# Kernel optimization log

Measured on AMD Instinct MI355X. Metric: run time of the kernel, lower is better.

The kernel has to match this reference:

```python
import jax, jax.numpy as jnp
import numpy as np

B, C, H, W = 32, 3, 224, 224
P = 14            # n_patches per side
PS = H // P       # 16
D = 768           # hidden_d
NH = 12           # n_heads
HD = D // NH      # 64
L = 12            # n_blocks
DFF = 4 * D
OUT = 1000
S = P * P + 1     # 197 tokens
EPS = 1e-5


def layernorm(x, g, b):
    m = jnp.mean(x, axis=-1, keepdims=True)
    v = jnp.mean(jnp.square(x - m), axis=-1, keepdims=True)
    return (x - m) * jax.lax.rsqrt(v + EPS) * g + b


def setup_inputs() -> dict:
    key = jax.random.key(0)
    ks = jax.random.split(key, 16)
    w = lambda k, shape: (jax.random.normal(k, shape, jnp.float32) * 0.02)
    inp = {
        'x': jax.random.normal(ks[0], (B, C, H, W), jnp.float32),
        'emb_w': w(ks[1], (C * PS * PS, D)),
        'emb_b': jnp.zeros((D,), jnp.float32),
        'cls': w(ks[2], (1, D)),
        'pos': w(ks[3], (S, D)),
        'pre_g': jnp.ones((D,), jnp.float32),
        'pre_b': jnp.zeros((D,), jnp.float32),
        'ln1_g': jnp.ones((L, D), jnp.float32),
        'ln1_b': jnp.zeros((L, D), jnp.float32),
        'qkv_w': w(ks[4], (L, D, 3 * D)),
        'qkv_b': jnp.zeros((L, 3 * D), jnp.float32),
        'proj_w': w(ks[5], (L, D, D)),
        'proj_b': jnp.zeros((L, D), jnp.float32),
        'ln2_g': jnp.ones((L, D), jnp.float32),
        'ln2_b': jnp.zeros((L, D), jnp.float32),
        'fc1_w': w(ks[6], (L, D, DFF)),
        'fc1_b': jnp.zeros((L, DFF), jnp.float32),
        'fc2_w': w(ks[7], (L, DFF, D)),
        'fc2_b': jnp.zeros((L, D), jnp.float32),
        'post_g': jnp.ones((D,), jnp.float32),
        'post_b': jnp.zeros((D,), jnp.float32),
        'head1_w': w(ks[8], (D, D)),
        'head1_b': jnp.zeros((D,), jnp.float32),
        'head2_w': w(ks[9], (D, OUT)),
        'head2_b': jnp.zeros((OUT,), jnp.float32),
    }
    return inp


def _forward(x, emb_w, emb_b, cls, pos, pre_g, pre_b,
             ln1_g, ln1_b, qkv_w, qkv_b, proj_w, proj_b,
             ln2_g, ln2_b, fc1_w, fc1_b, fc2_w, fc2_b,
             post_g, post_b, head1_w, head1_b, head2_w, head2_b):
    n = x.shape[0]
    # patchify: [n,C,H,W] -> [n, P*P, C*PS*PS] with flatten order (c, ph, pw)
    patches = x.reshape(n, C, P, PS, P, PS)
    patches = patches.transpose(0, 2, 4, 1, 3, 5).reshape(n, P * P, C * PS * PS)
    tokens = patches @ emb_w + emb_b                      # [n, P*P, D]
    tokens = jnp.concatenate([jnp.broadcast_to(cls[None], (n, 1, D)), tokens], axis=1)
    h = layernorm(tokens + pos[None], pre_g, pre_b)       # [n, S, D]

    scale = 1.0 / np.sqrt(HD)

    def block(h, p):
        g1, b1, qw, qb, pw, pb, g2, b2, f1w, f1b, f2w, f2b = p
        y = layernorm(h, g1, b1)
        qkv = (y @ qw + qb).reshape(n, S, 3, NH, HD).transpose(2, 0, 3, 1, 4)
        q, k, v = qkv[0], qkv[1], qkv[2]                  # [n, NH, S, HD]
        scores = jnp.einsum('bhsd,bhtd->bhst', q, k) * scale
        attn = jax.nn.softmax(scores, axis=-1)
        ctx = jnp.einsum('bhst,bhtd->bhsd', attn, v)
        ctx = ctx.transpose(0, 2, 1, 3).reshape(n, S, D)
        h = h + ctx @ pw + pb
        y = layernorm(h, g2, b2)
        mlp = jax.nn.gelu(y @ f1w + f1b, approximate=False) @ f2w + f2b
        return h + mlp, None

    h, _ = jax.lax.scan(block, h,
                        (ln1_g, ln1_b, qkv_w, qkv_b, proj_w, proj_b,
                         ln2_g, ln2_b, fc1_w, fc1_b, fc2_w, fc2_b))

    cls_out = layernorm(h[:, 0, :], post_g, post_b)
    preds = jnp.tanh(cls_out @ head1_w + head1_b) @ head2_w + head2_b
    return preds


def reference(x, emb_w, emb_b, cls, pos, pre_g, pre_b,
              ln1_g, ln1_b, qkv_w, qkv_b, proj_w, proj_b,
              ln2_g, ln2_b, fc1_w, fc1_b, fc2_w, fc2_b,
              post_g, post_b, head1_w, head1_b, head2_w, head2_b):
    return _forward(x, emb_w, emb_b, cls, pos, pre_g, pre_b,
                    ln1_g, ln1_b, qkv_w, qkv_b, proj_w, proj_b,
                    ln2_g, ln2_b, fc1_w, fc1_b, fc2_w, fc2_b,
                    post_g, post_b, head1_w, head1_b, head2_w, head2_b)
```

## Files before the change

### kernel.cpp

```cpp
#include <hip/hip_runtime.h>
#include <hip/hip_bf16.h>
#include <math.h>
#include <cstdint>

constexpr int Bn   = 32;
constexpr int Dn   = 768;
constexpr int NHn  = 12;
constexpr int HDn  = 64;
constexpr int Ln   = 12;
constexpr int DFFn = 3072;
constexpr int OUTn = 1000;
constexpr int Sn   = 197;
constexpr int Mrows = Bn * Sn;
constexpr int NPATCH = 196;

typedef __attribute__((ext_vector_type(8))) short bf16x8;
typedef __attribute__((ext_vector_type(4))) float f32x4;

__device__ inline void store_val(float* p, float v) { *p = v; }
__device__ inline void store_val(__hip_bfloat16* p, float v) { *p = __float2bfloat16(v); }
__device__ inline short f2bs(float f) {
  __hip_bfloat16 h = __float2bfloat16(f);
  return __builtin_bit_cast(short, h);
}

__device__ inline void gload_lds16(const void* g, void* l) {
  auto gp = (const __attribute__((address_space(1))) unsigned int*)(uintptr_t)g;
  auto lp = (__attribute__((address_space(3))) unsigned int*)(uintptr_t)l;
  __builtin_amdgcn_global_load_lds(gp, lp, 16, 0, 0);
}

__device__ inline int xcd_swizzle(int orig, int nwg) {
  const int xcd = orig & 7, local = orig >> 3;
  const int q = nwg >> 3, r = nwg & 7;
  return (xcd < r) ? xcd * (q + 1) + local : r * (q + 1) + (xcd - r) * q + local;
}

template<int ACT, bool RES, typename OT>
__global__ __launch_bounds__(256) void bgemm_kernel(
    const __hip_bfloat16* __restrict__ A,
    const __hip_bfloat16* __restrict__ Bt,
    const float* __restrict__ bias,
    const float* __restrict__ res,
    OT* __restrict__ out, int M, int N, int K)
{
  __shared__ __hip_bfloat16 As[3][128 * 32];
  __shared__ __hip_bfloat16 Bs[3][128 * 32];
  const int tid  = threadIdx.x;
  const int w    = tid >> 6, lane = tid & 63;
  const int wm   = w >> 1,   wn   = w & 1;
  const int kg   = lane >> 4, fr = lane & 15;

  const int nwg = gridDim.x * gridDim.y;
  const int wg  = xcd_swizzle(blockIdx.y * gridDim.x + blockIdx.x, nwg);
  const int bm  = (wg / gridDim.x) * 128;
  const int bn  = (wg % gridDim.x) * 128;

  const int obase0 = w * 2048;
  const int obase1 = w * 2048 + 1024;
  const int o0 = obase0 + lane * 16, o1 = obase1 + lane * 16;
  const int r0 = o0 >> 6,            r1 = o1 >> 6;
  const int ks0 = (((o0 >> 4) & 3) ^ (r0 & 3)) * 8;
  const int ks1 = (((o1 >> 4) & 3) ^ (r1 & 3)) * 8;
  const int ga0 = (bm + r0 >= M) ? M - 1 : bm + r0;
  const int ga1 = (bm + r1 >= M) ? M - 1 : bm + r1;
  const int gb0 = bn + r0, gb1 = bn + r1;

  f32x4 acc[4][4];
  #pragma unroll
  for (int i = 0; i < 4; ++i)
    #pragma unroll
    for (int j = 0; j < 4; ++j) acc[i][j] = (f32x4)(0.f);

  const int nt = K >> 5;

  auto STAGE = [&](int t, int bi) {
    const int k0 = t << 5;
    gload_lds16(A  + (size_t)ga0 * K + k0 + ks0, (char*)As[bi] + obase0);
    gload_lds16(A  + (size_t)ga1 * K + k0 + ks1, (char*)As[bi] + obase1);
    gload_lds16(Bt + (size_t)gb0 * K + k0 + ks0, (char*)Bs[bi] + obase0);
    gload_lds16(Bt + (size_t)gb1 * K + k0 + ks1, (char*)Bs[bi] + obase1);
  };
  auto COMPUTE = [&](int bi) {
    bf16x8 af[4], bfv[4];
    #pragma unroll
    for (int tt = 0; tt < 4; ++tt) {
      const int r = wm * 64 + tt * 16 + fr;
      af[tt]  = *(const bf16x8*)((const char*)As[bi] + r * 64 + ((kg ^ (r & 3)) << 4));
      const int c = wn * 64 + tt * 16 + fr;
      bfv[tt] = *(const bf16x8*)((const char*)Bs[bi] + c * 64 + ((kg ^ (c & 3)) << 4));
    }
    #pragma unroll
    for (int mt = 0; mt < 4; ++mt)
      #pragma unroll
      for (int nt2 = 0; nt2 < 4; ++nt2)
        acc[mt][nt2] = __builtin_amdgcn_mfma_f32_16x16x32_bf16(af[mt], bfv[nt2], acc[mt][nt2], 0, 0, 0);
  };

  STAGE(0, 0);
  STAGE(1, 1);

  int cur = 0;
  for (int t = 0; t < nt - 1; ++t) {
    asm volatile("s_waitcnt vmcnt(4)" ::: "memory");
    __builtin_amdgcn_s_barrier();
    __builtin_amdgcn_sched_barrier(0);
    if (t + 2 < nt) {
      int nb = cur + 2; if (nb >= 3) nb -= 3;
      STAGE(t + 2, nb);
    }
    COMPUTE(cur);
    ++cur; if (cur == 3) cur = 0;
  }
  asm volatile("s_waitcnt vmcnt(0)" ::: "memory");
  __builtin_amdgcn_s_barrier();
  __builtin_amdgcn_sched_barrier(0);
  COMPUTE(cur);

  #pragma unroll
  for (int nt2 = 0; nt2 < 4; ++nt2) {
    const int cb = bn + wn * 64 + nt2 * 16 + fr;
    const float bs = bias[cb];
    #pragma unroll
    for (int mt = 0; mt < 4; ++mt) {
      #pragma unroll
      for (int j = 0; j < 4; ++j) {
        const int rb = bm + wm * 64 + mt * 16 + kg * 4 + j;
        if (rb >= M) continue;
        float v = acc[mt][nt2][j] + bs;
        if (ACT == 1) v = 0.5f * v * (1.f + erff(v * 0.70710678118654752f));
        if (RES) v += res[(size_t)rb * N + cb];
        store_val(out + (size_t)rb * N + cb, v);
      }
    }
  }
}

template<int ACT, bool RES, typename OT>
__global__ __launch_bounds__(512) void wgemm_kernel(
    const __hip_bfloat16* __restrict__ A,
    const __hip_bfloat16* __restrict__ Bt,
    const float* __restrict__ bias,
    const float* __restrict__ res,
    OT* __restrict__ out, int M, int N, int K)
{
  constexpr int BUFSZ = 24576;
  __shared__ __align__(16) char lds[3 * BUFSZ];
  const int tid  = threadIdx.x;
  const int wid  = tid >> 6, lane = tid & 63;
  const int wm   = wid >> 2, wn = wid & 3;
  const int kg   = lane >> 4, fr = lane & 15;
  const int rs   = lane >> 2;
  const int ks   = (((lane & 3) ^ ((lane >> 2) & 3)) << 3);

  const int gx  = gridDim.x;
  const int nwg = gx * gridDim.y;
  const int wg  = xcd_swizzle(blockIdx.y * gx + blockIdx.x, nwg);
  const int bm  = (wg / gx) * 128;
  const int bn  = (wg % gx) * 256;

  f32x4 acc[4][4];
  #pragma unroll
  for (int i = 0; i < 4; ++i)
    #pragma unroll
    for (int j = 0; j < 4; ++j) acc[i][j] = (f32x4)(0.f);

  const int nt = K >> 5;

  auto STAGE = [&](int t) {
    const int k0 = t << 5;
    char* buf = lds + (t % 3) * BUFSZ;
    #pragma unroll
    for (int j = 0; j < 3; ++j) {
      const int c = wid + j * 8;
      const __hip_bfloat16* src;
      if (c < 8) {
        int gr = bm + c * 16 + rs; if (gr >= M) gr = M - 1;
        src = A + (size_t)gr * K + k0 + ks;
      } else {
        const int gc = bn + (c - 8) * 16 + rs;
        src = Bt + (size_t)gc * K + k0 + ks;
      }
      gload_lds16(src, buf + c * 1024);
    }
  };
  auto COMPUTE = [&](int t) {
    const char* buf = lds + (t % 3) * BUFSZ;
    bf16x8 af[4], bfv[4];
    #pragma unroll
    for (int tt = 0; tt < 4; ++tt) {
      const int r = wm * 64 + tt * 16 + fr;
      af[tt]  = *(const bf16x8*)(buf + r * 64 + ((kg ^ (r & 3)) << 4));
      const int c = wn * 64 + tt * 16 + fr;
      bfv[tt] = *(const bf16x8*)(buf + 8192 + c * 64 + ((kg ^ (c & 3)) << 4));
    }
    #pragma unroll
    for (int mt = 0; mt < 4; ++mt)
      #pragma unroll
      for (int nt2 = 0; nt2 < 4; ++nt2)
        acc[mt][nt2] = __builtin_amdgcn_mfma_f32_16x16x32_bf16(af[mt], bfv[nt2], acc[mt][nt2], 0, 0, 0);
  };

  STAGE(0);
  STAGE(1);

  for (int t = 0; t < nt - 1; ++t) {
    asm volatile("s_waitcnt vmcnt(3)" ::: "memory");
    __builtin_amdgcn_s_barrier();
    __builtin_amdgcn_sched_barrier(0);
    if (t + 2 < nt) STAGE(t + 2);
    COMPUTE(t);
  }
  asm volatile("s_waitcnt vmcnt(0)" ::: "memory");
  __builtin_amdgcn_s_barrier();
  __builtin_amdgcn_sched_barrier(0);
  COMPUTE(nt - 1);

  #pragma unroll
  for (int fj = 0; fj < 4; ++fj) {
    const int col = bn + wn * 64 + fj * 16 + fr;
    const float bs = bias[col];
    #pragma unroll
    for (int fi = 0; fi < 4; ++fi) {
      #pragma unroll
      for (int j = 0; j < 4; ++j) {
        const int row = bm + wm * 64 + fi * 16 + kg * 4 + j;
        if (row >= M) continue;
        float v = acc[fi][fj][j] + bs;
        if (ACT == 1) v = 0.5f * v * (1.f + erff(v * 0.70710678118654752f));
        if (RES) v += res[(size_t)row * N + col];
        store_val(out + (size_t)row * N + col, v);
      }
    }
  }
}

__global__ __launch_bounds__(256) void convT_kernel(const float* __restrict__ W,
                                                    __hip_bfloat16* __restrict__ Wt,
                                                    int K, int N)
{
  const size_t lw = (size_t)K * N;
  const float* Wb = W + blockIdx.z * lw;
  __hip_bfloat16* Wo = Wt + blockIdx.z * lw;
  __shared__ float t[32][33];
  const int k0 = blockIdx.y * 32, n0 = blockIdx.x * 32;
  const int r  = threadIdx.x >> 3, c4 = (threadIdx.x & 7) * 4;
  const float* wp = Wb + (size_t)(k0 + r) * N + n0 + c4;
  float4 v = make_float4(0.f, 0.f, 0.f, 0.f);
  if (n0 + c4 + 3 < N) v = *(const float4*)wp;
  else {
    if (n0 + c4 + 0 < N) v.x = wp[0];
    if (n0 + c4 + 1 < N) v.y = wp[1];
    if (n0 + c4 + 2 < N) v.z = wp[2];
  }
  t[r][c4 + 0] = v.x; t[r][c4 + 1] = v.y; t[r][c4 + 2] = v.z; t[r][c4 + 3] = v.w;
  __syncthreads();
  const int n = n0 + r;
  if (n < N) {
    __hip_bfloat16* o = Wo + (size_t)n * K + k0 + c4;
    o[0] = __float2bfloat16(t[c4 + 0][r]);
    o[1] = __float2bfloat16(t[c4 + 1][r]);
    o[2] = __float2bfloat16(t[c4 + 2][r]);
    o[3] = __float2bfloat16(t[c4 + 3][r]);
  }
}

template<int ACT>
__global__ __launch_bounds__(256) void hgemv_kernel(
    const float* __restrict__ A, const __hip_bfloat16* __restrict__ Wt,
    const float* __restrict__ bias, float* __restrict__ out, int N, int K)
{
  const int w = threadIdx.x >> 6, lane = threadIdx.x & 63;
  const int e = blockIdx.x * 4 + w;
  const int m = e & 31, n = e >> 5;
  if (n >= N) return;
  const float* a = A + (size_t)m * K;
  const __hip_bfloat16* wr = Wt + (size_t)n * K;
  float s = 0.f;
  for (int k = lane; k < K; k += 64)
    s = fmaf(a[k], __bfloat162float(wr[k]), s);
  #pragma unroll
  for (int o = 32; o > 0; o >>= 1) s += __shfl_xor(s, o);
  if (lane == 0) {
    float v = s + bias[n];
    if (ACT == 2) v = tanhf(v);
    out[(size_t)m * N + n] = v;
  }
}

__global__ __launch_bounds__(256) void patchify_kernel(const float* __restrict__ x,
                                                       __hip_bfloat16* __restrict__ p)
{
  size_t i = (size_t)blockIdx.x * 256 + threadIdx.x;
  constexpr size_t total = (size_t)Bn * NPATCH * 768;
  if (i >= total) return;
  int k = (int)(i % 768);
  size_t m = i / 768;
  int b = (int)(m / NPATCH), pp = (int)(m % NPATCH);
  int py = pp / 14, px = pp % 14;
  int c = k >> 8, ph = (k >> 4) & 15, pw = k & 15;
  p[i] = __float2bfloat16(x[(((size_t)(b * 3 + c)) * 224 + py * 16 + ph) * 224 + px * 16 + pw]);
}

__global__ __launch_bounds__(256) void assemble_kernel(const float* __restrict__ tok,
                                                       const float* __restrict__ cls,
                                                       const float* __restrict__ pos,
                                                       float* __restrict__ outp)
{
  size_t i = (size_t)blockIdx.x * 256 + threadIdx.x;
  constexpr size_t total = (size_t)Bn * Sn * Dn;
  if (i >= total) return;
  int d = (int)(i % Dn);
  size_t m = i / Dn;
  int s = (int)(m % Sn);
  size_t b = m / Sn;
  float v = (s == 0) ? cls[d] : tok[(b * NPATCH + (s - 1)) * Dn + d];
  outp[i] = v + pos[s * Dn + d];
}

template<typename OT>
__global__ __launch_bounds__(256) void ln_kernel(const float* __restrict__ x, size_t xstride,
                                                 const float* __restrict__ g,
                                                 const float* __restrict__ bt,
                                                 OT* __restrict__ out)
{
  const int row = blockIdx.x;
  const int tid = threadIdx.x;
  const float* xr = x + (size_t)row * xstride;
  float v0 = xr[tid], v1 = xr[tid + 256], v2 = xr[tid + 512];
  float s = v0 + v1 + v2;
  float q = v0 * v0 + v1 * v1 + v2 * v2;
  #pragma unroll
  for (int o = 32; o > 0; o >>= 1) { s += __shfl_down(s, o); q += __shfl_down(q, o); }
  __shared__ float sa[4], sb[4];
  int w = tid >> 6, lane = tid & 63;
  if (lane == 0) { sa[w] = s; sb[w] = q; }
  __syncthreads();
  if (tid == 0) {
    float ts = sa[0] + sa[1] + sa[2] + sa[3];
    float tq = sb[0] + sb[1] + sb[2] + sb[3];
    sa[0] = ts; sb[0] = tq;
  }
  __syncthreads();
  s = sa[0]; q = sb[0];
  const float mean = s * (1.f / 768.f);
  const float var  = q * (1.f / 768.f) - mean * mean;
  const float inv  = rsqrtf(var + 1e-5f);
  OT* orow = out + (size_t)row * Dn;
  store_val(orow + tid,       (v0 - mean) * inv * g[tid]       + bt[tid]);
  store_val(orow + tid + 256, (v1 - mean) * inv * g[tid + 256] + bt[tid + 256]);
  store_val(orow + tid + 512, (v2 - mean) * inv * g[tid + 512] + bt[tid + 512]);
}

constexpr int SP2 = 224;
constexpr int VTS = 232;
__global__ __launch_bounds__(256) void attn_mfma_kernel(
    const __hip_bfloat16* __restrict__ qkv, __hip_bfloat16* __restrict__ ctx)
{
  const int b = blockIdx.x / NHn, h = blockIdx.x % NHn;
  const int tid = threadIdx.x;
  const int w = tid >> 6, lane = tid & 63;
  const int kg = lane >> 4, fr = lane & 15;

  __shared__ short Kl[SP2 * 64];
  __shared__ short Vt[64 * VTS];
  __shared__ short Pl[4 * 2048];

  const size_t rstr = 3 * (size_t)Dn;
  const __hip_bfloat16* base = qkv + (size_t)b * Sn * rstr;

  #pragma unroll
  for (int it = 0; it < 7; ++it) {
    const int i = it * 256 + tid;
    const int r = i >> 3, s = i & 7;
    const int rr = r < Sn ? r : Sn - 1;
    gload_lds16(base + (size_t)rr * rstr + Dn + h * HDn + ((s ^ (r & 7)) << 3),
                (char*)Kl + it * 4096 + w * 1024);
  }
  #pragma unroll
  for (int it = 0; it < 7; ++it) {
    const int i = it * 256 + tid;
    const int key = i >> 3, d0 = (i & 7) * 8;
    const int rr = key < Sn ? key : Sn - 1;
    bf16x8 v = *(const bf16x8*)(base + (size_t)rr * rstr + 2 * Dn + h * HDn + d0);
    #pragma unroll
    for (int e = 0; e < 8; ++e) Vt[(d0 + e) * VTS + key] = v[e];
  }
  const int qw = w * 64;
  bf16x8 qf[4][2];
  #pragma unroll
  for (int qt = 0; qt < 4; ++qt)
    #pragma unroll
    for (int kk = 0; kk < 2; ++kk) {
      int q = qw + qt * 16 + fr; if (q >= Sn) q = Sn - 1;
      qf[qt][kk] = *(const bf16x8*)(base + (size_t)q * rstr + h * HDn + kk * 32 + kg * 8);
    }
  __syncthreads();

  float mold[4][4], lsum[4][4];
  f32x4 cacc[4][4];
  #pragma unroll
  for (int qt = 0; qt < 4; ++qt)
    #pragma unroll
    for (int j = 0; j < 4; ++j) {
      mold[qt][j] = -1e30f; lsum[qt][j] = 0.f;
      cacc[qt][j] = (f32x4)(0.f);
    }
  const float scale = 0.125f;

  for (int kc = 0; kc < SP2; kc += 32) {
    f32x4 sacc[4][2];
    #pragma unroll
    for (int qt = 0; qt < 4; ++qt) { sacc[qt][0] = (f32x4)(0.f); sacc[qt][1] = (f32x4)(0.f); }
    #pragma unroll
    for (int nt = 0; nt < 2; ++nt) {
      const int key = kc + nt * 16 + fr;
      const bf16x8 kf0 = *(const bf16x8*)((const char*)Kl + key * 128 + ((kg ^ (key & 7)) << 4));
      const bf16x8 kf1 = *(const bf16x8*)((const char*)Kl + key * 128 + (((4 + kg) ^ (key & 7)) << 4));
      #pragma unroll
      for (int qt = 0; qt < 4; ++qt) {
        sacc[qt][nt] = __builtin_amdgcn_mfma_f32_16x16x32_bf16(qf[qt][0], kf0, sacc[qt][nt], 0, 0, 0);
        sacc[qt][nt] = __builtin_amdgcn_mfma_f32_16x16x32_bf16(qf[qt][1], kf1, sacc[qt][nt], 0, 0, 0);
      }
    }
    const float madd0 = (kc + fr < Sn) ? 0.f : -3e38f;
    const float madd1 = (kc + 16 + fr < Sn) ? 0.f : -3e38f;
    #pragma unroll
    for (int qt = 0; qt < 4; ++qt) {
      sacc[qt][0] = sacc[qt][0] * scale + (f32x4)(madd0);
      sacc[qt][1] = sacc[qt][1] * scale + (f32x4)(madd1);
    }
    #pragma unroll
    for (int qt = 0; qt < 4; ++qt) {
      #pragma unroll
      for (int j = 0; j < 4; ++j) {
        float t = fmaxf(sacc[qt][0][j], sacc[qt][1][j]);
        t = fmaxf(t, __shfl_xor(t, 1));
        t = fmaxf(t, __shfl_xor(t, 2));
        t = fmaxf(t, __shfl_xor(t, 4));
        t = fmaxf(t, __shfl_xor(t, 8));
        const float mn = fmaxf(mold[qt][j], t);
        const float corr = __expf(mold[qt][j] - mn);
        mold[qt][j] = mn;
        const float p0 = __expf(sacc[qt][0][j] - mn);
        const float p1 = __expf(sacc[qt][1][j] - mn);
        sacc[qt][0][j] = p0; sacc[qt][1][j] = p1;
        float ps = p0 + p1;
        ps += __shfl_xor(ps, 1); ps += __shfl_xor(ps, 2);
        ps += __shfl_xor(ps, 4); ps += __shfl_xor(ps, 8);
        lsum[qt][j] = lsum[qt][j] * corr + ps;
        #pragma unroll
        for (int ht = 0; ht < 4; ++ht) cacc[qt][ht][j] *= corr;
      }
      #pragma unroll
      for (int nt = 0; nt < 2; ++nt) {
        const int c = nt * 16 + fr;
        #pragma unroll
        for (int j = 0; j < 4; ++j) {
          const int r = qt * 16 + kg * 4 + j;
          Pl[w * 2048 + r * 32 + (((c >> 3) ^ (r & 3)) << 3) + (c & 7)] = f2bs(sacc[qt][nt][j]);
        }
      }
    }
    bf16x8 vf[4];
    #pragma unroll
    for (int ht = 0; ht < 4; ++ht)
      vf[ht] = *(const bf16x8*)(Vt + (ht * 16 + fr) * VTS + kc + kg * 8);
    #pragma unroll
    for (int qt = 0; qt < 4; ++qt) {
      const int r = qt * 16 + fr;
      const bf16x8 pf = *(const bf16x8*)(Pl + w * 2048 + r * 32 + ((kg ^ (r & 3)) << 3));
      #pragma unroll
      for (int ht = 0; ht < 4; ++ht)
        cacc[qt][ht] = __builtin_amdgcn_mfma_f32_16x16x32_bf16(pf, vf[ht], cacc[qt][ht], 0, 0, 0);
    }
  }
  __hip_bfloat16* cb = ctx + (size_t)b * Sn * Dn + h * HDn;
  #pragma unroll
  for (int qt = 0; qt < 4; ++qt)
    #pragma unroll
    for (int j = 0; j < 4; ++j) {
      const int q = qw + qt * 16 + kg * 4 + j;
      if (q < Sn) {
        const float inv = 1.f / lsum[qt][j];
        #pragma unroll
        for (int ht = 0; ht < 4; ++ht)
          cb[(size_t)q * Dn + ht * 16 + fr] = __float2bfloat16(cacc[qt][ht][j] * inv);
      }
    }
}

using bf16 = __hip_bfloat16;

static inline void run_convT(const float* W, bf16* Wt, int K, int N, int L, hipStream_t st) {
  convT_kernel<<<dim3((N + 31) / 32, K / 32, L), 256, 0, st>>>(W, Wt, K, N);
}

extern "C" void kernel_launch(void* const* d_in, const int* in_sizes, int n_in,
                              void* d_out, int out_size, void* d_ws, size_t ws_size,
                              hipStream_t stream)
{
  const float* x      = (const float*)d_in[0];
  const float* emb_w  = (const float*)d_in[1];
  const float* emb_b  = (const float*)d_in[2];
  const float* cls    = (const float*)d_in[3];
  const float* pos    = (const float*)d_in[4];
  const float* pre_g  = (const float*)d_in[5];
  const float* pre_b  = (const float*)d_in[6];
  const float* ln1_g  = (const float*)d_in[7];
  const float* ln1_b  = (const float*)d_in[8];
  const float* qkv_w  = (const float*)d_in[9];
  const float* qkv_b  = (const float*)d_in[10];
  const float* proj_w = (const float*)d_in[11];
  const float* proj_b = (const float*)d_in[12];
  const float* ln2_g  = (const float*)d_in[13];
  const float* ln2_b  = (const float*)d_in[14];
  const float* fc1_w  = (const float*)d_in[15];
  const float* fc1_b  = (const float*)d_in[16];
  const float* fc2_w  = (const float*)d_in[17];
  const float* fc2_b  = (const float*)d_in[18];
  const float* post_g = (const float*)d_in[19];
  const float* post_b = (const float*)d_in[20];
  const float* h1_w   = (const float*)d_in[21];
  const float* h1_b   = (const float*)d_in[22];
  const float* h2_w   = (const float*)d_in[23];
  const float* h2_b   = (const float*)d_in[24];
  float* out = (float*)d_out;

  const size_t HN = (size_t)Mrows * Dn;
  float* hbuf = (float*)d_ws;
  bf16*  qkvb = (bf16*)(hbuf + HN);
  bf16*  abf1 = qkvb + (size_t)Mrows * 3 * Dn;
  bf16*  abf2 = abf1 + HN;
  bf16*  wtb  = abf2 + (size_t)Mrows * DFFn;

  bf16* bigq = wtb + (size_t)2304 * 768;
  bf16* bigp = bigq + (size_t)Ln * 3 * Dn * Dn;
  bf16* big1 = bigp + (size_t)Ln * Dn * Dn;
  bf16* big2 = big1 + (size_t)Ln * Dn * DFFn;
  const size_t need_big = (size_t)((char*)(big2 + (size_t)Ln * DFFn * Dn) - (char*)d_ws);
  const bool useBig = ws_size >= need_big;

  const int gM = (Mrows + 127) / 128;

  if (useBig) {
    run_convT(qkv_w,  bigq, Dn, 3 * Dn, Ln, stream);
    run_convT(proj_w, bigp, Dn, Dn,     Ln, stream);
    run_convT(fc1_w,  big1, Dn, DFFn,   Ln, stream);
    run_convT(fc2_w,  big2, DFFn, Dn,   Ln, stream);
  }

  patchify_kernel<<<(Bn * NPATCH * Dn) / 256, 256, 0, stream>>>(x, abf1);
  run_convT(emb_w, wtb, Dn, Dn, 1, stream);
  bgemm_kernel<0, false, float><<<dim3(Dn / 128, (Bn * NPATCH + 127) / 128), 256, 0, stream>>>(
      abf1, wtb, emb_b, nullptr, (float*)abf2, Bn * NPATCH, Dn, Dn);
  assemble_kernel<<<(Bn * Sn * Dn) / 256, 256, 0, stream>>>((float*)abf2, cls, pos, (float*)qkvb);
  ln_kernel<float><<<Mrows, 256, 0, stream>>>((float*)qkvb, (size_t)Dn, pre_g, pre_b, hbuf);

  for (int l = 0; l < Ln; ++l) {
    const float* g1 = ln1_g + (size_t)l * Dn;
    const float* b1 = ln1_b + (size_t)l * Dn;
    const float* qw = qkv_w + (size_t)l * Dn * 3 * Dn;
    const float* qb = qkv_b + (size_t)l * 3 * Dn;
    const float* pw = proj_w + (size_t)l * Dn * Dn;
    const float* pb = proj_b + (size_t)l * Dn;
    const float* g2 = ln2_g + (size_t)l * Dn;
    const float* b2 = ln2_b + (size_t)l * Dn;
    const float* f1w = fc1_w + (size_t)l * Dn * DFFn;
    const float* f1b = fc1_b + (size_t)l * DFFn;
    const float* f2w = fc2_w + (size_t)l * DFFn * Dn;
    const float* f2b = fc2_b + (size_t)l * Dn;

    const bf16* wq_t = useBig ? bigq + (size_t)l * 3 * Dn * Dn : wtb;
    const bf16* wp_t = useBig ? bigp + (size_t)l * Dn * Dn     : wtb;
    const bf16* w1_t = useBig ? big1 + (size_t)l * Dn * DFFn   : wtb;
    const bf16* w2_t = useBig ? big2 + (size_t)l * DFFn * Dn   : wtb;

    ln_kernel<bf16><<<Mrows, 256, 0, stream>>>(hbuf, (size_t)Dn, g1, b1, abf1);
    if (!useBig) run_convT(qw, wtb, Dn, 3 * Dn, 1, stream);
    wgemm_kernel<0, false, bf16><<<dim3(3 * Dn / 256, gM), 512, 0, stream>>>(
        abf1, wq_t, qb, nullptr, qkvb, Mrows, 3 * Dn, Dn);
    attn_mfma_kernel<<<Bn * NHn, 256, 0, stream>>>(qkvb, abf1);
    if (!useBig) run_convT(pw, wtb, Dn, Dn, 1, stream);
    bgemm_kernel<0, true, float><<<dim3(Dn / 128, gM), 256, 0, stream>>>(
        abf1, wp_t, pb, hbuf, hbuf, Mrows, Dn, Dn);
    ln_kernel<bf16><<<Mrows, 256, 0, stream>>>(hbuf, (size_t)Dn, g2, b2, abf1);
    if (!useBig) run_convT(f1w, wtb, Dn, DFFn, 1, stream);
    wgemm_kernel<1, false, bf16><<<dim3(DFFn / 256, gM), 512, 0, stream>>>(
        abf1, w1_t, f1b, nullptr, abf2, Mrows, DFFn, Dn);
    if (!useBig) run_convT(f2w, wtb, DFFn, Dn, 1, stream);
    bgemm_kernel<0, true, float><<<dim3(Dn / 128, gM), 256, 0, stream>>>(
        abf2, w2_t, f2b, hbuf, hbuf, Mrows, Dn, DFFn);
  }

  float* t1 = (float*)abf2;
  float* t2 = t1 + Bn * Dn;
  ln_kernel<float><<<Bn, 256, 0, stream>>>(hbuf, (size_t)Sn * Dn, post_g, post_b, t1);
  run_convT(h1_w, wtb, Dn, Dn, 1, stream);
  hgemv_kernel<2><<<Bn * Dn / 4, 256, 0, stream>>>(t1, wtb, h1_b, t2, Dn, Dn);
  run_convT(h2_w, wtb, Dn, OUTn, 1, stream);
  hgemv_kernel<0><<<Bn * OUTn / 4, 256, 0, stream>>>(t2, wtb, h2_b, out, OUTn, Dn);
}
```

Before: 3.311 ms.

## Use 256x256 tiles with K=64 double-buffered LDS for QKV and FC1 GEMMs

Replaces the 128x256 triple-buffered K=32 wide GEMM with a 256x256 tile kernel that uses K=64 steps, a 128 KB double-buffered LDS, and a new XOR swizzle. The next tile's global-to-LDS loads are interleaved in quarters between MFMA groups, with s_setprio raising priority during the MFMA sections. The goal is more data reuse per loaded byte and better overlap of memory traffic with matrix math. The cost is fewer workgroups (fewer M tiles, so more tail waste for M=6304), higher register use for 32 accumulators, and extra barriers per K step.

```diff
diff --git a/kernel.cpp b/kernel.cpp
--- a/kernel.cpp
+++ b/kernel.cpp
@@ -137,94 +137,111 @@
 }
 
 template<int ACT, bool RES, typename OT>
-__global__ __launch_bounds__(512) void wgemm_kernel(
+__global__ __launch_bounds__(512) void wgemm256_kernel(
     const __hip_bfloat16* __restrict__ A,
     const __hip_bfloat16* __restrict__ Bt,
     const float* __restrict__ bias,
     const float* __restrict__ res,
     OT* __restrict__ out, int M, int N, int K)
 {
-  constexpr int BUFSZ = 24576;
-  __shared__ __align__(16) char lds[3 * BUFSZ];
+  constexpr int BUF = 65536;
+  __shared__ __align__(16) char lds[2 * BUF];
   const int tid  = threadIdx.x;
   const int wid  = tid >> 6, lane = tid & 63;
   const int wm   = wid >> 2, wn = wid & 3;
   const int kg   = lane >> 4, fr = lane & 15;
-  const int rs   = lane >> 2;
-  const int ks   = (((lane & 3) ^ ((lane >> 2) & 3)) << 3);
+  const int srow = lane >> 3;
+  const int sks  = ((lane & 7) * 8) ^ ((lane >> 5) * 16);
 
   const int gx  = gridDim.x;
   const int nwg = gx * gridDim.y;
   const int wg  = xcd_swizzle(blockIdx.y * gx + blockIdx.x, nwg);
-  const int bm  = (wg / gx) * 128;
+  const int bm  = (wg / gx) * 256;
   const int bn  = (wg % gx) * 256;
 
-  f32x4 acc[4][4];
-  #pragma unroll
-  for (int i = 0; i < 4; ++i)
+  f32x4 acc[8][4];
+  #pragma unroll
+  for (int i = 0; i < 8; ++i)
     #pragma unroll
     for (int j = 0; j < 4; ++j) acc[i][j] = (f32x4)(0.f);
 
-  const int nt = K >> 5;
-
-  auto STAGE = [&](int t) {
-    const int k0 = t << 5;
-    char* buf = lds + (t % 3) * BUFSZ;
-    #pragma unroll
-    for (int j = 0; j < 3; ++j) {
-      const int c = wid + j * 8;
-      const __hip_bfloat16* src;
-      if (c < 8) {
-        int gr = bm + c * 16 + rs; if (gr >= M) gr = M - 1;
-        src = A + (size_t)gr * K + k0 + ks;
+  const int nt = K >> 6;
+
+  auto STAGE2 = [&](int t, int q) {
+    const int kbase = t << 6;
+    char* buf = lds + (t & 1) * BUF;
+    #pragma unroll
+    for (int j = 0; j < 2; ++j) {
+      const int c = q * 16 + j * 8 + wid;
+      if (c < 32) {
+        int gr = bm + c * 8 + srow; if (gr >= M) gr = M - 1;
+        gload_lds16(A + (size_t)gr * K + kbase + sks, buf + c * 1024);
       } else {
-        const int gc = bn + (c - 8) * 16 + rs;
-        src = Bt + (size_t)gc * K + k0 + ks;
-      }
-      gload_lds16(src, buf + c * 1024);
+        const int gc = bn + (c - 32) * 8 + srow;
+        gload_lds16(Bt + (size_t)gc * K + kbase + sks, buf + c * 1024);
+      }
     }
   };
-  auto COMPUTE = [&](int t) {
-    const char* buf = lds + (t % 3) * BUFSZ;
-    bf16x8 af[4], bfv[4];
-    #pragma unroll
-    for (int tt = 0; tt < 4; ++tt) {
-      const int r = wm * 64 + tt * 16 + fr;
-      af[tt]  = *(const bf16x8*)(buf + r * 64 + ((kg ^ (r & 3)) << 4));
-      const int c = wn * 64 + tt * 16 + fr;
-      bfv[tt] = *(const bf16x8*)(buf + 8192 + c * 64 + ((kg ^ (c & 3)) << 4));
-    }
-    #pragma unroll
-    for (int mt = 0; mt < 4; ++mt)
-      #pragma unroll
-      for (int nt2 = 0; nt2 < 4; ++nt2)
-        acc[mt][nt2] = __builtin_amdgcn_mfma_f32_16x16x32_bf16(af[mt], bfv[nt2], acc[mt][nt2], 0, 0, 0);
-  };
-
-  STAGE(0);
-  STAGE(1);
-
-  for (int t = 0; t < nt - 1; ++t) {
-    asm volatile("s_waitcnt vmcnt(3)" ::: "memory");
+
+  STAGE2(0, 0); STAGE2(0, 1); STAGE2(0, 2); STAGE2(0, 3);
+
+  for (int t = 0; t < nt; ++t) {
+    asm volatile("s_waitcnt vmcnt(0)" ::: "memory");
     __builtin_amdgcn_s_barrier();
     __builtin_amdgcn_sched_barrier(0);
-    if (t + 2 < nt) STAGE(t + 2);
-    COMPUTE(t);
-  }
-  asm volatile("s_waitcnt vmcnt(0)" ::: "memory");
-  __builtin_amdgcn_s_barrier();
-  __builtin_amdgcn_sched_barrier(0);
-  COMPUTE(nt - 1);
+    const char* buf = lds + (t & 1) * BUF;
+    const bool stg = (t + 1 < nt);
+
+    bf16x8 bf[4][2];
+    #pragma unroll
+    for (int fj = 0; fj < 4; ++fj)
+      #pragma unroll
+      for (int kh = 0; kh < 2; ++kh) {
+        const int c = wn * 64 + fj * 16 + fr;
+        int byte = 32768 + c * 128 + kh * 64 + kg * 16;
+        byte ^= ((c >> 2) & 1) << 5;
+        bf[fj][kh] = *(const bf16x8*)(buf + byte);
+      }
+
+    #pragma unroll
+    for (int q = 0; q < 4; ++q) {
+      bf16x8 af[2][2];
+      #pragma unroll
+      for (int fi = 0; fi < 2; ++fi)
+        #pragma unroll
+        for (int kh = 0; kh < 2; ++kh) {
+          const int r = wm * 128 + (q * 2 + fi) * 16 + fr;
+          int byte = r * 128 + kh * 64 + kg * 16;
+          byte ^= ((r >> 2) & 1) << 5;
+          af[fi][kh] = *(const bf16x8*)(buf + byte);
+        }
+      if (stg) STAGE2(t + 1, q);
+      __builtin_amdgcn_sched_barrier(0);
+      __builtin_amdgcn_s_barrier();
+      __builtin_amdgcn_s_setprio(1);
+      #pragma unroll
+      for (int kh = 0; kh < 2; ++kh)
+        #pragma unroll
+        for (int fi = 0; fi < 2; ++fi)
+          #pragma unroll
+          for (int fj = 0; fj < 4; ++fj)
+            acc[q * 2 + fi][fj] = __builtin_amdgcn_mfma_f32_16x16x32_bf16(
+                af[fi][kh], bf[fj][kh], acc[q * 2 + fi][fj], 0, 0, 0);
+      __builtin_amdgcn_s_setprio(0);
+      __builtin_amdgcn_sched_barrier(0);
+      __builtin_amdgcn_s_barrier();
+    }
+  }
 
   #pragma unroll
   for (int fj = 0; fj < 4; ++fj) {
     const int col = bn + wn * 64 + fj * 16 + fr;
     const float bs = bias[col];
     #pragma unroll
-    for (int fi = 0; fi < 4; ++fi) {
+    for (int fi = 0; fi < 8; ++fi) {
       #pragma unroll
       for (int j = 0; j < 4; ++j) {
-        const int row = bm + wm * 64 + fi * 16 + kg * 4 + j;
+        const int row = bm + wm * 128 + fi * 16 + kg * 4 + j;
         if (row >= M) continue;
         float v = acc[fi][fj][j] + bs;
         if (ACT == 1) v = 0.5f * v * (1.f + erff(v * 0.70710678118654752f));
@@ -541,7 +558,8 @@
   const size_t need_big = (size_t)((char*)(big2 + (size_t)Ln * DFFn * Dn) - (char*)d_ws);
   const bool useBig = ws_size >= need_big;
 
-  const int gM = (Mrows + 127) / 128;
+  const int gM   = (Mrows + 127) / 128;
+  const int gM2  = (Mrows + 255) / 256;
 
   if (useBig) {
     run_convT(qkv_w,  bigq, Dn, 3 * Dn, Ln, stream);
@@ -578,7 +596,7 @@
 
     ln_kernel<bf16><<<Mrows, 256, 0, stream>>>(hbuf, (size_t)Dn, g1, b1, abf1);
     if (!useBig) run_convT(qw, wtb, Dn, 3 * Dn, 1, stream);
-    wgemm_kernel<0, false, bf16><<<dim3(3 * Dn / 256, gM), 512, 0, stream>>>(
+    wgemm256_kernel<0, false, bf16><<<dim3(3 * Dn / 256, gM2), 512, 0, stream>>>(
         abf1, wq_t, qb, nullptr, qkvb, Mrows, 3 * Dn, Dn);
     attn_mfma_kernel<<<Bn * NHn, 256, 0, stream>>>(qkvb, abf1);
     if (!useBig) run_convT(pw, wtb, Dn, Dn, 1, stream);
@@ -586,7 +604,7 @@
         abf1, wp_t, pb, hbuf, hbuf, Mrows, Dn, Dn);
     ln_kernel<bf16><<<Mrows, 256, 0, stream>>>(hbuf, (size_t)Dn, g2, b2, abf1);
     if (!useBig) run_convT(f1w, wtb, Dn, DFFn, 1, stream);
-    wgemm_kernel<1, false, bf16><<<dim3(DFFn / 256, gM), 512, 0, stream>>>(
+    wgemm256_kernel<1, false, bf16><<<dim3(DFFn / 256, gM2), 512, 0, stream>>>(
         abf1, w1_t, f1b, nullptr, abf2, Mrows, DFFn, Dn);
     if (!useBig) run_convT(f2w, wtb, DFFn, Dn, 1, stream);
     bgemm_kernel<0, true, float><<<dim3(Dn / 128, gM), 256, 0, stream>>>(
```

After: 3.938 ms. 19.0% more time.
